# Optimization experiments

Measured on AMD Instinct MI355X. Metric: run time of the kernel, lower is better.

## Reference

```python
import jax, jax.numpy as jnp
import numpy as np

N_HEAD = 16
N_KV_HEAD = 4
HEAD_DIM = 128
SOFT_CAP = 50.0
ROPE_BASE = 10000.0
RMS_EPS = 1e-6


def rmsnorm(x, w):
    # normalize over last dim (head_dim)
    var = jnp.mean(x * x, axis=-1, keepdims=True)
    return x * jax.lax.rsqrt(var + RMS_EPS) * w


def rope_cos_sin(T, dtype):
    inv_freq = 1.0 / (ROPE_BASE ** (jnp.arange(0, HEAD_DIM, 2, dtype=jnp.float32) / HEAD_DIM))
    t = jnp.arange(T, dtype=jnp.float32)
    freqs = jnp.outer(t, inv_freq)  # [T, HEAD_DIM//2]
    return jnp.cos(freqs).astype(dtype), jnp.sin(freqs).astype(dtype)


def apply_rotary(x, cos, sin):
    # x: [B, T, H, D]; cos/sin: [T, D//2] broadcast as [1, T, 1, D//2]
    d = x.shape[-1] // 2
    x1, x2 = x[..., :d], x[..., d:]
    c = cos[None, :, None, :]
    s = sin[None, :, None, :]
    y1 = x1 * c + x2 * s
    y2 = -x1 * s + x2 * c
    return jnp.concatenate([y1, y2], axis=-1)


def setup_inputs() -> dict:
    key = jax.random.key(0)
    ks = jax.random.split(key, 6)
    B, T, C = 1, 4096, 2048
    sc = 1.0 / np.sqrt(C)
    return {
        "x": jax.random.normal(ks[0], (B, T, C), jnp.float32),
        "Wq": jax.random.normal(ks[1], (C, C), jnp.float32) * sc,
        "Wkv": jax.random.normal(ks[2], (C, 2 * N_KV_HEAD * HEAD_DIM), jnp.float32) * sc,
        "Wc": jax.random.normal(ks[3], (C, C), jnp.float32) * sc,
        "qn_w": jnp.ones((HEAD_DIM,), jnp.float32),
        "kn_w": jnp.ones((HEAD_DIM,), jnp.float32),
    }


def reference(x, Wq, Wkv, Wc, qn_w, kn_w):
    B, T, C = x.shape
    g = N_HEAD // N_KV_HEAD  # GQA group size

    q = (x @ Wq).reshape(B, T, N_HEAD, HEAD_DIM)
    kv = (x @ Wkv).reshape(B, T, 2, N_KV_HEAD, HEAD_DIM)
    k, v = kv[:, :, 0], kv[:, :, 1]

    q = rmsnorm(q, qn_w)
    k = rmsnorm(k, kn_w)

    cos, sin = rope_cos_sin(T, x.dtype)
    q = apply_rotary(q, cos, sin)
    k = apply_rotary(k, cos, sin)

    # [B, H, T, D]
    q = q.transpose(0, 2, 1, 3)
    k = k.transpose(0, 2, 1, 3)
    v = v.transpose(0, 2, 1, 3)
    # repeat_interleave K/V to emulate GQA
    k = jnp.repeat(k, g, axis=1)
    v = jnp.repeat(v, g, axis=1)

    att = jnp.einsum("bhqd,bhkd->bhqk", q, k) / np.sqrt(HEAD_DIM)
    att = SOFT_CAP * jnp.tanh(att / SOFT_CAP)  # soft logit capping
    causal = jnp.tril(jnp.ones((T, T), dtype=bool))
    att = jnp.where(causal[None, None], att, -jnp.inf)
    att = jax.nn.softmax(att, axis=-1)

    y = jnp.einsum("bhqk,bhkd->bhqd", att, v)
    y = y.transpose(0, 2, 1, 3).reshape(B, T, C)
    return y @ Wc
```

## Files before the change

kernel.cpp:

```cpp
#include <hip/hip_runtime.h>
#include <hip/hip_bf16.h>
#include <math.h>

#define T_SEQ 4096
#define C_DIM 2048
#define NH 16
#define NKV 4
#define HD 128

typedef __attribute__((ext_vector_type(4))) float f32x4;
typedef __attribute__((ext_vector_type(16))) float f32x16;
typedef __attribute__((ext_vector_type(8))) short s16x8;
typedef __hip_bfloat16 bf16;

typedef __attribute__((address_space(3))) void lds_void;
typedef __attribute__((address_space(1))) const void gbl_void;
#define ASYNC16(g, l) __builtin_amdgcn_global_load_lds((gbl_void*)(g), (lds_void*)(l), 16, 0, 0)

__device__ __forceinline__ float cap_exp(float s) {
  float t = __expf(s * 0.04f);
  float r = __builtin_amdgcn_rcpf(t + 1.0f);
  return __expf(__fmaf_rn(r, -100.0f, 50.0f));
}

__device__ __forceinline__ unsigned packbf(float a, float b) {
  unsigned ua = (unsigned)__bfloat16_as_ushort(__float2bfloat16(a));
  unsigned ub = (unsigned)__bfloat16_as_ushort(__float2bfloat16(b));
  return ua | (ub << 16);
}

__global__ void k_cvt_bf16(const float* __restrict__ in, bf16* __restrict__ out, int n4) {
  int i = blockIdx.x * blockDim.x + threadIdx.x;
  if (i < n4) {
    float4 v = ((const float4*)in)[i];
    union { bf16 h[4]; short4 s; } u;
    u.h[0] = __float2bfloat16(v.x);
    u.h[1] = __float2bfloat16(v.y);
    u.h[2] = __float2bfloat16(v.z);
    u.h[3] = __float2bfloat16(v.w);
    ((short4*)out)[i] = u.s;
  }
}

__global__ void k_transpose_cvt(const float* __restrict__ in, bf16* __restrict__ out,
                                int K, int N) {
  __shared__ float tile[64][65];
  int n0 = blockIdx.x * 64, k0 = blockIdx.y * 64;
  int c = threadIdx.x & 63, r0 = threadIdx.x >> 6;
#pragma unroll
  for (int it = 0; it < 16; ++it) {
    int r = it * 4 + r0;
    tile[r][c] = in[(size_t)(k0 + r) * N + (n0 + c)];
  }
  __syncthreads();
#pragma unroll
  for (int it = 0; it < 16; ++it) {
    int r = it * 4 + r0;
    out[(size_t)(n0 + r) * K + (k0 + c)] = __float2bfloat16(tile[c][r]);
  }
}

__global__ __launch_bounds__(256) void k_gemm_bt(
    const bf16* __restrict__ A, const bf16* __restrict__ Bt, float* __restrict__ C,
    int M, int N, int K) {
  __shared__ __align__(16) bf16 As[128 * 64];
  __shared__ __align__(16) bf16 Bs[128 * 64];
  int nTilesN = N >> 7;
  int bm = blockIdx.x / nTilesN, bn = blockIdx.x % nTilesN;
  int row0 = bm * 128, col0 = bn * 128;
  int tid = threadIdx.x, lane = tid & 63, wid = tid >> 6;
  int wm = wid >> 1, wn = wid & 1;
  int l15 = lane & 15, l4 = lane >> 4;
  f32x4 acc[4][4] = {};
  int srow = lane >> 3;
  int schk = lane & 7;
  for (int kt = 0; kt < (K >> 6); ++kt) {
    const bf16* Ab = A + (size_t)row0 * K + kt * 64;
    const bf16* Bb = Bt + (size_t)col0 * K + kt * 64;
#pragma unroll
    for (int it = 0; it < 4; ++it) {
      int t = wid * 4 + it;
      ASYNC16(Ab + (size_t)(8 * t + srow) * K + schk * 8, As + t * 512);
      ASYNC16(Bb + (size_t)(8 * t + srow) * K + schk * 8, Bs + t * 512);
    }
    __syncthreads();
#pragma unroll
    for (int ks = 0; ks < 2; ++ks) {
      s16x8 af[4], bfr[4];
#pragma unroll
      for (int m = 0; m < 4; ++m)
        af[m] = *(const s16x8*)(As + (wm * 64 + m * 16 + l15) * 64 + ks * 32 + l4 * 8);
#pragma unroll
      for (int n = 0; n < 4; ++n)
        bfr[n] = *(const s16x8*)(Bs + (wn * 64 + n * 16 + l15) * 64 + ks * 32 + l4 * 8);
#pragma unroll
      for (int m = 0; m < 4; ++m)
#pragma unroll
        for (int n = 0; n < 4; ++n)
          acc[m][n] = __builtin_amdgcn_mfma_f32_16x16x32_bf16(af[m], bfr[n], acc[m][n], 0, 0, 0);
    }
    __syncthreads();
  }
#pragma unroll
  for (int m = 0; m < 4; ++m)
#pragma unroll
    for (int n = 0; n < 4; ++n)
#pragma unroll
      for (int r = 0; r < 4; ++r) {
        int rr = row0 + wm * 64 + m * 16 + l4 * 4 + r;
        int cc = col0 + wn * 64 + n * 16 + l15;
        C[(size_t)rr * N + cc] = acc[m][n][r];
      }
}

__global__ void k_qkprep(const float* __restrict__ src, int rowStride, int nh,
                         const float* __restrict__ w, float outScale,
                         bf16* __restrict__ out) {
  int idx = blockIdx.x * 4 + (threadIdx.x >> 6);
  int lane = threadIdx.x & 63;
  int t = idx / nh;
  int h = idx & (nh - 1);
  const float* s = src + (size_t)t * rowStride + h * HD;
  float x1 = s[lane], x2 = s[lane + 64];
  float ss = x1 * x1 + x2 * x2;
#pragma unroll
  for (int m = 1; m < 64; m <<= 1) ss += __shfl_xor(ss, m);
  float rs = rsqrtf(ss * (1.0f / 128.0f) + 1e-6f);
  x1 *= rs * w[lane];
  x2 *= rs * w[lane + 64];
  float invf = expf(-(float)lane * 0.14391156831212787f);
  float fr = (float)t * invf;
  float sv, cv;
  sincosf(fr, &sv, &cv);
  float y1 = (x1 * cv + x2 * sv) * outScale;
  float y2 = (-x1 * sv + x2 * cv) * outScale;
  bf16* dst = out + ((size_t)h * T_SEQ + t) * HD;
  dst[lane] = __float2bfloat16(y1);
  dst[lane + 64] = __float2bfloat16(y2);
}

__global__ void k_vtrans(const float* __restrict__ kv32, bf16* __restrict__ Vt) {
  __shared__ float tile[64][65];
  int t0 = blockIdx.x * 64, d0 = blockIdx.y * 64, hk = blockIdx.z;
  int c = threadIdx.x & 63, r0 = threadIdx.x >> 6;
#pragma unroll
  for (int it = 0; it < 16; ++it) {
    int r = it * 4 + r0;
    tile[r][c] = kv32[(size_t)(t0 + r) * 1024 + 512 + hk * 128 + d0 + c];
  }
  __syncthreads();
#pragma unroll
  for (int it = 0; it < 16; ++it) {
    int r = it * 4 + r0;
    Vt[((size_t)hk * 128 + d0 + r) * T_SEQ + (t0 + c)] = __float2bfloat16(tile[c][r]);
  }
}

__global__ __launch_bounds__(256) void k_attn2(
    const bf16* __restrict__ Qb, const bf16* __restrict__ Kb,
    const bf16* __restrict__ Vt, bf16* __restrict__ Y) {
  __shared__ __align__(16) bf16 Ks[64 * 128];
  __shared__ __align__(16) bf16 Vs[128 * 64];
  __shared__ float sInv[4][32];
  int bx = blockIdx.x;
  int qb = 31 - (bx >> 4);
  int h = bx & 15;
  int hk = h >> 2;
  int tid = threadIdx.x, lane = tid & 63, w = tid >> 6;
  int l31 = lane & 31, hi = lane >> 5;
  int qrow0b = qb * 128;
  int qrow0w = qrow0b + w * 32;
  int wqmax = qrow0w + 31;

  const bf16* Kbase = Kb + (size_t)hk * T_SEQ * HD;
  const bf16* Vbase = Vt + (size_t)hk * HD * T_SEQ;

  s16x8 qf[8];
  {
    const bf16* Qp = Qb + ((size_t)h * T_SEQ + qrow0w + l31) * HD + hi * 8;
#pragma unroll
    for (int s = 0; s < 8; ++s) qf[s] = *(const s16x8*)(Qp + s * 16);
  }
  f32x16 acc[4] = {};
  float lp = 0.f;

  int nt = qrow0b / 64 + 2;
  for (int kt = 0; kt < nt; ++kt) {
    int kv0 = kt * 64;
#pragma unroll
    for (int i = 0; i < 4; ++i) {
      int j = w * 4 + i;
      int rk = j * 4 + (lane >> 4);
      int chk = (lane & 15) ^ (rk & 15);
      ASYNC16(Kbase + (size_t)(kv0 + rk) * HD + chk * 8, Ks + j * 512);
      int dv = j * 8 + (lane >> 3);
      int chv = (lane & 7) ^ (dv & 7);
      ASYNC16(Vbase + (size_t)dv * T_SEQ + kv0 + chv * 8, Vs + j * 512);
    }
    __syncthreads();
#pragma unroll
    for (int sub = 0; sub < 2; ++sub) {
      int kv0s = kv0 + sub * 32;
      if (kv0s <= wqmax) {
        f32x16 sacc = {};
#pragma unroll
        for (int s = 0; s < 8; ++s) {
          int r = sub * 32 + l31;
          s16x8 kf = *(const s16x8*)(Ks + r * 128 + (((2 * s + hi) ^ (r & 15)) * 8));
          sacc = __builtin_amdgcn_mfma_f32_32x32x16_bf16(kf, qf[s], sacc, 0, 0, 0);
        }
        float p[16];
        bool needmask = (kv0s + 31 > qrow0w);
        int qidx = qrow0w + l31;
#pragma unroll
        for (int r = 0; r < 16; ++r) {
          int kvl = (r & 3) + 8 * (r >> 2) + 4 * hi;
          float pe = cap_exp(sacc[r]);
          if (needmask) pe = (kv0s + kvl > qidx) ? 0.f : pe;
          p[r] = pe;
          lp += pe;
        }
        unsigned u[8];
#pragma unroll
        for (int i2 = 0; i2 < 8; ++i2) u[i2] = packbf(p[2 * i2], p[2 * i2 + 1]);
        s16x8 pa[2];
#pragma unroll
        for (int s2 = 0; s2 < 2; ++s2) {
          int b = s2 * 4;
          unsigned t0 = (unsigned)__shfl_xor((int)u[b + 0], 32);
          unsigned t1 = (unsigned)__shfl_xor((int)u[b + 1], 32);
          unsigned t2 = (unsigned)__shfl_xor((int)u[b + 2], 32);
          unsigned t3 = (unsigned)__shfl_xor((int)u[b + 3], 32);
          union { unsigned wd[4]; s16x8 v; } cv;
          cv.wd[0] = hi ? t2 : u[b + 0];
          cv.wd[1] = hi ? t3 : u[b + 1];
          cv.wd[2] = hi ? u[b + 2] : t0;
          cv.wd[3] = hi ? u[b + 3] : t1;
          pa[s2] = cv.v;
        }
#pragma unroll
        for (int db = 0; db < 4; ++db) {
          int d = db * 32 + l31;
#pragma unroll
          for (int s2 = 0; s2 < 2; ++s2) {
            int lch = sub * 4 + s2 * 2 + hi;
            s16x8 vf = *(const s16x8*)(Vs + d * 64 + ((lch ^ (d & 7)) * 8));
            acc[db] = __builtin_amdgcn_mfma_f32_32x32x16_bf16(pa[s2], vf, acc[db], 0, 0, 0);
          }
        }
      }
    }
    __syncthreads();
  }
  float ltot = lp + __shfl_xor(lp, 32);
  if (hi == 0) sInv[w][l31] = 1.0f / ltot;
#pragma unroll
  for (int db = 0; db < 4; ++db) {
#pragma unroll
    for (int r = 0; r < 16; ++r) {
      int qrow = (r & 3) + 8 * (r >> 2) + 4 * hi;
      float val = acc[db][r] * sInv[w][qrow];
      Y[(size_t)(qrow0w + qrow) * C_DIM + h * HD + db * 32 + l31] = __float2bfloat16(val);
    }
  }
}

extern "C" void kernel_launch(void* const* d_in, const int* in_sizes, int n_in,
                              void* d_out, int out_size, void* d_ws, size_t ws_size,
                              hipStream_t stream) {
  const float* x = (const float*)d_in[0];
  const float* Wq = (const float*)d_in[1];
  const float* Wkv = (const float*)d_in[2];
  const float* Wc = (const float*)d_in[3];
  const float* qnw = (const float*)d_in[4];
  const float* knw = (const float*)d_in[5];
  float* out = (float*)d_out;

  char* ws = (char*)d_ws;
  size_t off = 0;
  auto alloc = [&](size_t b) { void* p = ws + off; off += (b + 255) & ~(size_t)255; return p; };

  bf16* xb = (bf16*)alloc((size_t)T_SEQ * C_DIM * 2);
  bf16* WqT = (bf16*)alloc((size_t)C_DIM * C_DIM * 2);
  bf16* WkvT = (bf16*)alloc((size_t)1024 * C_DIM * 2);
  bf16* WcT = (bf16*)alloc((size_t)C_DIM * C_DIM * 2);
  float* kv32 = (float*)alloc((size_t)T_SEQ * 1024 * 4);
  bf16* Qb = (bf16*)alloc((size_t)NH * T_SEQ * HD * 2);
  bf16* Kb = (bf16*)alloc((size_t)NKV * T_SEQ * HD * 2);
  bf16* Vt = (bf16*)alloc((size_t)NKV * HD * T_SEQ * 2);
  bf16* Yb = (bf16*)alloc((size_t)T_SEQ * C_DIM * 2);
  float* q32 = out;

  k_cvt_bf16<<<(T_SEQ * C_DIM / 4 + 255) / 256, 256, 0, stream>>>(x, xb, T_SEQ * C_DIM / 4);
  k_transpose_cvt<<<dim3(C_DIM / 64, C_DIM / 64), 256, 0, stream>>>(Wq, WqT, C_DIM, C_DIM);
  k_transpose_cvt<<<dim3(1024 / 64, C_DIM / 64), 256, 0, stream>>>(Wkv, WkvT, C_DIM, 1024);
  k_transpose_cvt<<<dim3(C_DIM / 64, C_DIM / 64), 256, 0, stream>>>(Wc, WcT, C_DIM, C_DIM);

  k_gemm_bt<<<(T_SEQ / 128) * (C_DIM / 128), 256, 0, stream>>>(xb, WqT, q32, T_SEQ, C_DIM, C_DIM);
  k_gemm_bt<<<(T_SEQ / 128) * (1024 / 128), 256, 0, stream>>>(xb, WkvT, kv32, T_SEQ, 1024, C_DIM);

  k_qkprep<<<T_SEQ * NH / 4, 256, 0, stream>>>(q32, C_DIM, NH, qnw, 0.08838834764831845f, Qb);
  k_qkprep<<<T_SEQ * NKV / 4, 256, 0, stream>>>(kv32, 1024, NKV, knw, 1.0f, Kb);
  k_vtrans<<<dim3(T_SEQ / 64, 2, NKV), 256, 0, stream>>>(kv32, Vt);

  k_attn2<<<dim3(512), 256, 0, stream>>>(Qb, Kb, Vt, Yb);

  k_gemm_bt<<<(T_SEQ / 128) * (C_DIM / 128), 256, 0, stream>>>(Yb, WcT, out, T_SEQ, C_DIM, C_DIM);
}
```

Measured before the change: 455.7 us.

## Split attention KV across warp pairs, fuse QKV GEMMs, precompute RoPE table

New measurement: 438.2 us. 3.9% less time.

```diff
diff --git a/kernel.cpp b/kernel.cpp
--- a/kernel.cpp
+++ b/kernel.cpp
@@ -60,8 +60,20 @@
   }
 }
 
+__global__ void k_rope_table(float* __restrict__ ctab, float* __restrict__ stab) {
+  int idx = blockIdx.x * blockDim.x + threadIdx.x;
+  int t = idx >> 6, i = idx & 63;
+  float invf = __expf(-(float)i * 0.14391156831212787f);
+  float fr = (float)t * invf;
+  float sv, cv;
+  __sincosf(fr, &sv, &cv);
+  ctab[idx] = cv;
+  stab[idx] = sv;
+}
+
 __global__ __launch_bounds__(256) void k_gemm_bt(
-    const bf16* __restrict__ A, const bf16* __restrict__ Bt, float* __restrict__ C,
+    const bf16* __restrict__ A, const bf16* __restrict__ Bt,
+    float* __restrict__ Cq, int ldq, float* __restrict__ Ckv, int ldkv, int split,
     int M, int N, int K) {
   __shared__ __align__(16) bf16 As[128 * 64];
   __shared__ __align__(16) bf16 Bs[128 * 64];
@@ -101,6 +113,10 @@
     }
     __syncthreads();
   }
+  float* Cbase;
+  int ldc, ccoff;
+  if (col0 < split) { Cbase = Cq; ldc = ldq; ccoff = 0; }
+  else { Cbase = Ckv; ldc = ldkv; ccoff = split; }
 #pragma unroll
   for (int m = 0; m < 4; ++m)
 #pragma unroll
@@ -108,13 +124,14 @@
 #pragma unroll
       for (int r = 0; r < 4; ++r) {
         int rr = row0 + wm * 64 + m * 16 + l4 * 4 + r;
-        int cc = col0 + wn * 64 + n * 16 + l15;
-        C[(size_t)rr * N + cc] = acc[m][n][r];
+        int cc = col0 + wn * 64 + n * 16 + l15 - ccoff;
+        Cbase[(size_t)rr * ldc + cc] = acc[m][n][r];
       }
 }
 
 __global__ void k_qkprep(const float* __restrict__ src, int rowStride, int nh,
                          const float* __restrict__ w, float outScale,
+                         const float* __restrict__ ctab, const float* __restrict__ stab,
                          bf16* __restrict__ out) {
   int idx = blockIdx.x * 4 + (threadIdx.x >> 6);
   int lane = threadIdx.x & 63;
@@ -128,10 +145,7 @@
   float rs = rsqrtf(ss * (1.0f / 128.0f) + 1e-6f);
   x1 *= rs * w[lane];
   x2 *= rs * w[lane + 64];
-  float invf = expf(-(float)lane * 0.14391156831212787f);
-  float fr = (float)t * invf;
-  float sv, cv;
-  sincosf(fr, &sv, &cv);
+  float cv = ctab[t * 64 + lane], sv = stab[t * 64 + lane];
   float y1 = (x1 * cv + x2 * sv) * outScale;
   float y2 = (-x1 * sv + x2 * cv) * outScale;
   bf16* dst = out + ((size_t)h * T_SEQ + t) * HD;
@@ -156,37 +170,42 @@
   }
 }
 
-__global__ __launch_bounds__(256) void k_attn2(
+union AttnLds {
+  struct { __align__(16) bf16 K[64 * 128]; __align__(16) bf16 V[128 * 64]; } st;
+  float mrg[2][64 * 65];
+};
+__global__ __launch_bounds__(256) void k_attn3(
     const bf16* __restrict__ Qb, const bf16* __restrict__ Kb,
     const bf16* __restrict__ Vt, bf16* __restrict__ Y) {
-  __shared__ __align__(16) bf16 Ks[64 * 128];
-  __shared__ __align__(16) bf16 Vs[128 * 64];
-  __shared__ float sInv[4][32];
+  __shared__ AttnLds lds;
+  __shared__ float lpbuf[2][32];
+  __shared__ float invbuf[2][32];
   int bx = blockIdx.x;
-  int qb = 31 - (bx >> 4);
+  int qb = 63 - (bx >> 4);
   int h = bx & 15;
   int hk = h >> 2;
   int tid = threadIdx.x, lane = tid & 63, w = tid >> 6;
   int l31 = lane & 31, hi = lane >> 5;
-  int qrow0b = qb * 128;
-  int qrow0w = qrow0b + w * 32;
-  int wqmax = qrow0w + 31;
-
+  int qsub = w >> 1, p = w & 1;
+  int q0 = qb * 64;
+  int qw0 = q0 + qsub * 32;
+
+  bf16* Ks = lds.st.K;
+  bf16* Vs = lds.st.V;
   const bf16* Kbase = Kb + (size_t)hk * T_SEQ * HD;
   const bf16* Vbase = Vt + (size_t)hk * HD * T_SEQ;
 
   s16x8 qf[8];
   {
-    const bf16* Qp = Qb + ((size_t)h * T_SEQ + qrow0w + l31) * HD + hi * 8;
+    const bf16* Qp = Qb + ((size_t)h * T_SEQ + qw0 + l31) * HD + hi * 8;
 #pragma unroll
     for (int s = 0; s < 8; ++s) qf[s] = *(const s16x8*)(Qp + s * 16);
   }
   f32x16 acc[4] = {};
   float lp = 0.f;
 
-  int nt = qrow0b / 64 + 2;
-  for (int kt = 0; kt < nt; ++kt) {
-    int kv0 = kt * 64;
+  for (int jj = 0; jj <= qb; ++jj) {
+    int kv0 = jj * 64;
 #pragma unroll
     for (int i = 0; i < 4; ++i) {
       int j = w * 4 + i;
@@ -198,70 +217,77 @@
       ASYNC16(Vbase + (size_t)dv * T_SEQ + kv0 + chv * 8, Vs + j * 512);
     }
     __syncthreads();
-#pragma unroll
-    for (int sub = 0; sub < 2; ++sub) {
-      int kv0s = kv0 + sub * 32;
-      if (kv0s <= wqmax) {
-        f32x16 sacc = {};
-#pragma unroll
-        for (int s = 0; s < 8; ++s) {
-          int r = sub * 32 + l31;
-          s16x8 kf = *(const s16x8*)(Ks + r * 128 + (((2 * s + hi) ^ (r & 15)) * 8));
-          sacc = __builtin_amdgcn_mfma_f32_32x32x16_bf16(kf, qf[s], sacc, 0, 0, 0);
-        }
-        float p[16];
-        bool needmask = (kv0s + 31 > qrow0w);
-        int qidx = qrow0w + l31;
-#pragma unroll
-        for (int r = 0; r < 16; ++r) {
-          int kvl = (r & 3) + 8 * (r >> 2) + 4 * hi;
-          float pe = cap_exp(sacc[r]);
-          if (needmask) pe = (kv0s + kvl > qidx) ? 0.f : pe;
-          p[r] = pe;
-          lp += pe;
-        }
-        unsigned u[8];
-#pragma unroll
-        for (int i2 = 0; i2 < 8; ++i2) u[i2] = packbf(p[2 * i2], p[2 * i2 + 1]);
-        s16x8 pa[2];
+    int kvs = kv0 + p * 32;
+    if (kvs <= qw0 + 31) {
+      f32x16 sacc = {};
+      int r = p * 32 + l31;
+#pragma unroll
+      for (int s = 0; s < 8; ++s) {
+        s16x8 kf = *(const s16x8*)(Ks + r * 128 + (((2 * s + hi) ^ (r & 15)) * 8));
+        sacc = __builtin_amdgcn_mfma_f32_32x32x16_bf16(kf, qf[s], sacc, 0, 0, 0);
+      }
+      float pv[16];
+      bool needmask = (kvs == qw0);
+#pragma unroll
+      for (int rr = 0; rr < 16; ++rr) {
+        int kvl = (rr & 3) + 8 * (rr >> 2) + 4 * hi;
+        float pe = cap_exp(sacc[rr]);
+        if (needmask) pe = (kvl > l31) ? 0.f : pe;
+        pv[rr] = pe;
+        lp += pe;
+      }
+      unsigned u[8];
+#pragma unroll
+      for (int i2 = 0; i2 < 8; ++i2) u[i2] = packbf(pv[2 * i2], pv[2 * i2 + 1]);
+      s16x8 pa[2];
+#pragma unroll
+      for (int s2 = 0; s2 < 2; ++s2) {
+        int b = s2 * 4;
+        unsigned t0 = (unsigned)__shfl_xor((int)u[b + 0], 32);
+        unsigned t1 = (unsigned)__shfl_xor((int)u[b + 1], 32);
+        unsigned t2 = (unsigned)__shfl_xor((int)u[b + 2], 32);
+        unsigned t3 = (unsigned)__shfl_xor((int)u[b + 3], 32);
+        union { unsigned wd[4]; s16x8 v; } cv;
+        cv.wd[0] = hi ? t2 : u[b + 0];
+        cv.wd[1] = hi ? t3 : u[b + 1];
+        cv.wd[2] = hi ? u[b + 2] : t0;
+        cv.wd[3] = hi ? u[b + 3] : t1;
+        pa[s2] = cv.v;
+      }
+#pragma unroll
+      for (int db = 0; db < 4; ++db) {
+        int d = db * 32 + l31;
 #pragma unroll
         for (int s2 = 0; s2 < 2; ++s2) {
-          int b = s2 * 4;
-          unsigned t0 = (unsigned)__shfl_xor((int)u[b + 0], 32);
-          unsigned t1 = (unsigned)__shfl_xor((int)u[b + 1], 32);
-          unsigned t2 = (unsigned)__shfl_xor((int)u[b + 2], 32);
-          unsigned t3 = (unsigned)__shfl_xor((int)u[b + 3], 32);
-          union { unsigned wd[4]; s16x8 v; } cv;
-          cv.wd[0] = hi ? t2 : u[b + 0];
-          cv.wd[1] = hi ? t3 : u[b + 1];
-          cv.wd[2] = hi ? u[b + 2] : t0;
-          cv.wd[3] = hi ? u[b + 3] : t1;
-          pa[s2] = cv.v;
-        }
-#pragma unroll
-        for (int db = 0; db < 4; ++db) {
-          int d = db * 32 + l31;
-#pragma unroll
-          for (int s2 = 0; s2 < 2; ++s2) {
-            int lch = sub * 4 + s2 * 2 + hi;
-            s16x8 vf = *(const s16x8*)(Vs + d * 64 + ((lch ^ (d & 7)) * 8));
-            acc[db] = __builtin_amdgcn_mfma_f32_32x32x16_bf16(pa[s2], vf, acc[db], 0, 0, 0);
-          }
+          int lch = p * 4 + s2 * 2 + hi;
+          s16x8 vf = *(const s16x8*)(Vs + d * 64 + ((lch ^ (d & 7)) * 8));
+          acc[db] = __builtin_amdgcn_mfma_f32_32x32x16_bf16(pa[s2], vf, acc[db], 0, 0, 0);
         }
       }
     }
     __syncthreads();
   }
-  float ltot = lp + __shfl_xor(lp, 32);
-  if (hi == 0) sInv[w][l31] = 1.0f / ltot;
-#pragma unroll
-  for (int db = 0; db < 4; ++db) {
-#pragma unroll
-    for (int r = 0; r < 16; ++r) {
-      int qrow = (r & 3) + 8 * (r >> 2) + 4 * hi;
-      float val = acc[db][r] * sInv[w][qrow];
-      Y[(size_t)(qrow0w + qrow) * C_DIM + h * HD + db * 32 + l31] = __float2bfloat16(val);
-    }
+  float lps = lp + __shfl_xor(lp, 32);
+  if (p == 1) {
+    if (hi == 0) lpbuf[qsub][l31] = lps;
+#pragma unroll
+    for (int db = 0; db < 4; ++db)
+#pragma unroll
+      for (int rr = 0; rr < 16; ++rr)
+        lds.mrg[qsub][lane * 65 + db * 16 + rr] = acc[db][rr];
+  }
+  __syncthreads();
+  if (p == 0) {
+    float ltot = lps + lpbuf[qsub][l31];
+    if (hi == 0) invbuf[qsub][l31] = 1.0f / ltot;
+#pragma unroll
+    for (int db = 0; db < 4; ++db)
+#pragma unroll
+      for (int rr = 0; rr < 16; ++rr) {
+        int qrow = (rr & 3) + 8 * (rr >> 2) + 4 * hi;
+        float val = (acc[db][rr] + lds.mrg[qsub][lane * 65 + db * 16 + rr]) * invbuf[qsub][qrow];
+        Y[(size_t)(qw0 + qrow) * C_DIM + h * HD + db * 32 + l31] = __float2bfloat16(val);
+      }
   }
 }
 
@@ -289,21 +315,25 @@
   bf16* Kb = (bf16*)alloc((size_t)NKV * T_SEQ * HD * 2);
   bf16* Vt = (bf16*)alloc((size_t)NKV * HD * T_SEQ * 2);
   bf16* Yb = (bf16*)alloc((size_t)T_SEQ * C_DIM * 2);
+  float* ctab = (float*)alloc((size_t)T_SEQ * 64 * 4);
+  float* stab = (float*)alloc((size_t)T_SEQ * 64 * 4);
   float* q32 = out;
 
   k_cvt_bf16<<<(T_SEQ * C_DIM / 4 + 255) / 256, 256, 0, stream>>>(x, xb, T_SEQ * C_DIM / 4);
   k_transpose_cvt<<<dim3(C_DIM / 64, C_DIM / 64), 256, 0, stream>>>(Wq, WqT, C_DIM, C_DIM);
   k_transpose_cvt<<<dim3(1024 / 64, C_DIM / 64), 256, 0, stream>>>(Wkv, WkvT, C_DIM, 1024);
   k_transpose_cvt<<<dim3(C_DIM / 64, C_DIM / 64), 256, 0, stream>>>(Wc, WcT, C_DIM, C_DIM);
-
-  k_gemm_bt<<<(T_SEQ / 128) * (C_DIM / 128), 256, 0, stream>>>(xb, WqT, q32, T_SEQ, C_DIM, C_DIM);
-  k_gemm_bt<<<(T_SEQ / 128) * (1024 / 128), 256, 0, stream>>>(xb, WkvT, kv32, T_SEQ, 1024, C_DIM);
-
-  k_qkprep<<<T_SEQ * NH / 4, 256, 0, stream>>>(q32, C_DIM, NH, qnw, 0.08838834764831845f, Qb);
-  k_qkprep<<<T_SEQ * NKV / 4, 256, 0, stream>>>(kv32, 1024, NKV, knw, 1.0f, Kb);
+  k_rope_table<<<T_SEQ * 64 / 256, 256, 0, stream>>>(ctab, stab);
+
+  k_gemm_bt<<<(T_SEQ / 128) * (3072 / 128), 256, 0, stream>>>(
+      xb, WqT, q32, C_DIM, kv32, 1024, C_DIM, T_SEQ, 3072, C_DIM);
+
+  k_qkprep<<<T_SEQ * NH / 4, 256, 0, stream>>>(q32, C_DIM, NH, qnw, 0.08838834764831845f, ctab, stab, Qb);
+  k_qkprep<<<T_SEQ * NKV / 4, 256, 0, stream>>>(kv32, 1024, NKV, knw, 1.0f, ctab, stab, Kb);
   k_vtrans<<<dim3(T_SEQ / 64, 2, NKV), 256, 0, stream>>>(kv32, Vt);
 
-  k_attn2<<<dim3(512), 256, 0, stream>>>(Qb, Kb, Vt, Yb);
-
-  k_gemm_bt<<<(T_SEQ / 128) * (C_DIM / 128), 256, 0, stream>>>(Yb, WcT, out, T_SEQ, C_DIM, C_DIM);
-}
+  k_attn3<<<dim3(1024), 256, 0, stream>>>(Qb, Kb, Vt, Yb);
+
+  k_gemm_bt<<<(T_SEQ / 128) * (C_DIM / 128), 256, 0, stream>>>(
+      Yb, WcT, out, C_DIM, nullptr, 0, C_DIM, T_SEQ, C_DIM, C_DIM);
+}
```
